# Kernel tuning notes

Hardware: AMD Instinct MI355X
Metric: run time of the kernel (lower is better)

The kernel has to match this reference:

```python
import jax, jax.numpy as jnp
import numpy as np

B, T, D_MODEL = 2, 2048, 2048
H, HD = 16, 128          # num_heads, head_dim
KV_L, Q_L, R = 512, 1024, 64  # kv_latent, q_latent, qk_rope_dim


def apply_rope(x, freqs):
    # x: (..., T, R); freqs: (T, R//2) angles theta (torch stores exp(i*theta))
    # torch pairs consecutive elements: view(..., R//2, 2) as complex
    xr = x.reshape(x.shape[:-1] + (R // 2, 2))
    x0, x1 = xr[..., 0], xr[..., 1]
    cos, sin = jnp.cos(freqs), jnp.sin(freqs)  # broadcast over leading dims
    y0 = x0 * cos - x1 * sin
    y1 = x0 * sin + x1 * cos
    return jnp.stack([y0, y1], axis=-1).reshape(x.shape)


def setup_inputs() -> dict:
    key = jax.random.key(0)
    ks = jax.random.split(key, 10)
    s = 0.02
    return {
        "x": jax.random.normal(ks[0], (B, T, D_MODEL), jnp.float32),
        "freqs": jax.random.normal(ks[1], (T, R // 2), jnp.float32),
        # weights stored as (in, out) so forward is x @ W (== torch x @ W.T)
        "W_DKV": jax.random.normal(ks[2], (D_MODEL, KV_L), jnp.float32) * s,
        "W_UK": jax.random.normal(ks[3], (KV_L, H * HD), jnp.float32) * s,
        "W_UV": jax.random.normal(ks[4], (KV_L, H * HD), jnp.float32) * s,
        "W_KR": jax.random.normal(ks[5], (D_MODEL, R), jnp.float32) * s,
        "W_DQ": jax.random.normal(ks[6], (D_MODEL, Q_L), jnp.float32) * s,
        "W_UQ": jax.random.normal(ks[7], (Q_L, H * HD), jnp.float32) * s,
        "W_QR": jax.random.normal(ks[8], (Q_L, H * R), jnp.float32) * s,
        "W_O": jax.random.normal(ks[9], (H * HD, D_MODEL), jnp.float32) * s,
    }


def reference(x, freqs, W_DKV, W_UK, W_UV, W_KR, W_DQ, W_UQ, W_QR, W_O):
    b, t, _ = x.shape
    # compressed KV latent and expansions
    c_KV = x @ W_DKV                                             # (B,T,KV_L)
    K_c = (c_KV @ W_UK).reshape(b, t, H, HD).transpose(0, 2, 1, 3)  # (B,H,T,HD)
    V = (c_KV @ W_UV).reshape(b, t, H, HD).transpose(0, 2, 1, 3)    # (B,H,T,HD)
    # shared (single-head) rope key
    K_r1 = apply_rope((x @ W_KR)[:, None, :, :], freqs)          # (B,1,T,R)
    K_r = jnp.broadcast_to(K_r1, (b, H, t, R))
    # compressed Q latent
    c_Q = x @ W_DQ                                               # (B,T,Q_L)
    Q_c = (c_Q @ W_UQ).reshape(b, t, H, HD).transpose(0, 2, 1, 3)
    Q_r = apply_rope((c_Q @ W_QR).reshape(b, t, H, R).transpose(0, 2, 1, 3), freqs)
    Q = jnp.concatenate([Q_c, Q_r], axis=-1)                     # (B,H,T,HD+R)
    K = jnp.concatenate([K_c, K_r], axis=-1)
    # causal SDPA, scale = 1/sqrt(HD+R) (torch default: query last dim)
    scale = 1.0 / jnp.sqrt(jnp.asarray(HD + R, Q.dtype))
    scores = jnp.einsum("bhqe,bhke->bhqk", Q, K) * scale
    causal = jnp.tril(jnp.ones((t, t), bool))
    scores = jnp.where(causal, scores, jnp.asarray(-1e30, scores.dtype))
    attn = jax.nn.softmax(scores, axis=-1)
    out = jnp.einsum("bhqk,bhkd->bhqd", attn, V)                 # (B,H,T,HD)
    out = out.transpose(0, 2, 1, 3).reshape(b, t, H * HD)
    y = out @ W_O                                                # (B,T,D_MODEL)
    return (y, c_KV, K_r1[:, 0, :, :])
```

## Files before the change

kernel.cpp:

```cpp
#include <hip/hip_runtime.h>
#include <stdint.h>

typedef unsigned short u16;
typedef __attribute__((ext_vector_type(8))) short s16x8;
typedef __attribute__((ext_vector_type(4))) float f32x4;

#define B_   2
#define T_   2048
#define DM   2048
#define H_   16
#define HD_  128
#define R_   64
#define E_   192
#define SCALE2 0.104117542f

__device__ __forceinline__ u16 f2b(float f) {
  union { float f; uint32_t u; } x; x.f = f;
  uint32_t u = x.u;
  return (u16)((u + 0x7FFFu + ((u >> 16) & 1u)) >> 16);
}
__device__ __forceinline__ float b2f(u16 h) {
  union { uint32_t u; float f; } x; x.u = ((uint32_t)h) << 16;
  return x.f;
}
__device__ __forceinline__ unsigned pk2(float a, float b) {
  union { float f; unsigned u; } A, B; A.f = a; B.f = b;
  return (B.u & 0xFFFF0000u) | (A.u >> 16);
}
__device__ __forceinline__ void ld_lds16(const void* g, void* l) {
  __builtin_amdgcn_global_load_lds((const __attribute__((address_space(1))) void*)g,
                                   (__attribute__((address_space(3))) void*)l,
                                   16, 0, 0);
}

__device__ __forceinline__ void conv_dev(const float* __restrict__ in, u16* __restrict__ out, int i) {
  float4 v = *(const float4*)(in + (size_t)i * 4);
  ushort4 o;
  o.x = f2b(v.x); o.y = f2b(v.y); o.z = f2b(v.z); o.w = f2b(v.w);
  *(ushort4*)(out + (size_t)i * 4) = o;
}
__device__ __forceinline__ void tr64(const float* __restrict__ in, u16* __restrict__ out,
                                     int K, int N, int bx, int by) {
  __shared__ u16 t[64][65];
  int bn = bx * 64, bk = by * 64;
  int tid = threadIdx.x;
  int r0 = tid >> 4, c0 = (tid & 15) * 4;
#pragma unroll
  for (int rr = 0; rr < 64; rr += 16) {
    float4 v = *(const float4*)(in + (size_t)(bk + r0 + rr) * N + bn + c0);
    t[r0 + rr][c0 + 0] = f2b(v.x); t[r0 + rr][c0 + 1] = f2b(v.y);
    t[r0 + rr][c0 + 2] = f2b(v.z); t[r0 + rr][c0 + 3] = f2b(v.w);
  }
  __syncthreads();
#pragma unroll
  for (int rr = 0; rr < 64; rr += 16) {
    ushort4 v;
    v.x = t[c0 + 0][r0 + rr]; v.y = t[c0 + 1][r0 + rr];
    v.z = t[c0 + 2][r0 + rr]; v.w = t[c0 + 3][r0 + rr];
    *(ushort4*)(out + (size_t)(bn + r0 + rr) * K + bk + c0) = v;
  }
}

__global__ __launch_bounds__(256)
void ta_k(const float* __restrict__ x, const float* __restrict__ fr,
          u16* __restrict__ x_bf, u16* __restrict__ fr_bf,
          const float* __restrict__ wdkv, const float* __restrict__ wkr,
          const float* __restrict__ wdq, u16* __restrict__ W) {
  int id = blockIdx.x;
  if (id < 8192)        conv_dev(x, x_bf, id * 256 + threadIdx.x);
  else if (id < 8256)   conv_dev(fr, fr_bf, (id - 8192) * 256 + threadIdx.x);
  else if (id < 8512) { int i = id - 8256; tr64(wdkv, W, 2048, 512, i & 7, i >> 3); }
  else if (id < 8544) { int i = id - 8512; tr64(wkr, W + 512 * 2048, 2048, 64, 0, i); }
  else                { int i = id - 8544; tr64(wdq, W + 576 * 2048, 2048, 1024, i & 15, i >> 4); }
}
__global__ __launch_bounds__(256)
void tb1_k(const float* __restrict__ wuk, const float* __restrict__ wuv, u16* __restrict__ W) {
  int id = blockIdx.x;
  if (id < 256) tr64(wuk, W, 512, 2048, id & 31, id >> 5);
  else { int i = id - 256; tr64(wuv, W + 2048 * 512, 512, 2048, i & 31, i >> 5); }
}
__global__ __launch_bounds__(256)
void tb2_k(const float* __restrict__ wuq, const float* __restrict__ wqr, u16* __restrict__ W) {
  int id = blockIdx.x;
  if (id < 512) tr64(wuq, W, 1024, 2048, id & 31, id >> 5);
  else { int i = id - 512; tr64(wqr, W + 2048 * 1024, 1024, 1024, i & 15, i >> 4); }
}
__global__ __launch_bounds__(256)
void tc_k(const float* __restrict__ wo, u16* __restrict__ W) {
  tr64(wo, W, 2048, 2048, blockIdx.x & 31, blockIdx.x >> 5);
}

template <int EPI>
__global__ __launch_bounds__(256)
void gemm_bf16(const u16* __restrict__ A, const u16* __restrict__ Bt,
               u16* __restrict__ O0, u16* __restrict__ O1, u16* __restrict__ O2,
               float* __restrict__ OF, float* __restrict__ OF2,
               const u16* __restrict__ FR, int M, int N, int K) {
  __shared__ __align__(16) u16 Al[128 * 32];
  __shared__ __align__(16) u16 Bl[128 * 32];
  const int tid = threadIdx.x;
  const int ln = tid & 63, w = tid >> 6;
  const int quad = ln >> 4, l16 = ln & 15;
  const int wm = (w >> 1) * 64, wn = (w & 1) * 64;
  const int m0 = blockIdx.y * 128, n0 = blockIdx.x * 128;

  f32x4 zz = {0.f, 0.f, 0.f, 0.f};
  f32x4 acc[4][4];
#pragma unroll
  for (int i = 0; i < 4; i++)
#pragma unroll
    for (int j = 0; j < 4; j++) acc[i][j] = zz;

  const u16* aG[2];
  const u16* bG[2];
  int ldsC[2];
#pragma unroll
  for (int r = 0; r < 2; r++) {
    int i = tid + r * 256;
    int row = i >> 2, cq = (i & 3) * 8;
    aG[r] = A + (size_t)(m0 + row) * K + cq;
    int rb = n0 + row;
    if (rb > N - 1) rb = N - 1;
    bG[r] = Bt + (size_t)rb * K + cq;
    ldsC[r] = ((tid & ~63) + r * 256) * 8;
  }

  for (int k = 0; k < K; k += 32) {
#pragma unroll
    for (int r = 0; r < 2; r++) {
      ld_lds16(aG[r] + k, &Al[ldsC[r]]);
      ld_lds16(bG[r] + k, &Bl[ldsC[r]]);
    }
    __syncthreads();
    s16x8 af[4], bf[4];
#pragma unroll
    for (int f = 0; f < 4; f++)
      af[f] = *(const s16x8*)&Al[(wm + f * 16 + l16) * 32 + quad * 8];
#pragma unroll
    for (int f = 0; f < 4; f++)
      bf[f] = *(const s16x8*)&Bl[(wn + f * 16 + l16) * 32 + quad * 8];
#pragma unroll
    for (int i = 0; i < 4; i++)
#pragma unroll
      for (int j = 0; j < 4; j++)
        acc[i][j] = __builtin_amdgcn_mfma_f32_16x16x32_bf16(af[i], bf[j], acc[i][j], 0, 0, 0);
    __syncthreads();
  }

#pragma unroll
  for (int fm = 0; fm < 4; fm++) {
#pragma unroll
    for (int fn = 0; fn < 4; fn++) {
      int n = n0 + wn + fn * 16 + l16;
      int mb = m0 + wm + fm * 16 + quad * 4;
      if (EPI == 2) {
        if (n < N) {
#pragma unroll
          for (int rg = 0; rg < 4; rg++) OF[(size_t)(mb + rg) * N + n] = acc[fm][fn][rg];
        }
      } else if (EPI == 4) {
        if (n < 2048) {
#pragma unroll
          for (int rg = 0; rg < 4; rg++) O0[(size_t)(mb + rg) * 2048 + n] = f2b(acc[fm][fn][rg]);
        } else {
          int hd = n - 2048, b = mb >> 11, t = mb & 2047;
          ushort4 v;
          v.x = f2b(acc[fm][fn][0]); v.y = f2b(acc[fm][fn][1]);
          v.z = f2b(acc[fm][fn][2]); v.w = f2b(acc[fm][fn][3]);
          *(ushort4*)(O1 + ((size_t)(b * 2048 + hd) * 2048 + t)) = v;
        }
      } else if (EPI == 5) {
        if (n < 2048) {
#pragma unroll
          for (int rg = 0; rg < 4; rg++) O0[(size_t)(mb + rg) * 2048 + n] = f2b(acc[fm][fn][rg]);
        } else {
#pragma unroll
          for (int rg = 0; rg < 4; rg++) O1[(size_t)(mb + rg) * 1024 + (n - 2048)] = f2b(acc[fm][fn][rg]);
        }
      } else {
        if (n < 512) {
#pragma unroll
          for (int rg = 0; rg < 4; rg++) {
            float v = acc[fm][fn][rg];
            O0[(size_t)(mb + rg) * 512 + n] = f2b(v);
            OF[(size_t)(mb + rg) * 512 + n] = v;
          }
        } else if (n < 576) {
          int r = n - 512, r2 = r >> 1, odd = r & 1;
#pragma unroll
          for (int rg = 0; rg < 4; rg++) {
            float v = acc[fm][fn][rg];
            float p = __shfl_xor(v, 1);
            int t = mb + rg;
            float a = b2f(FR[(size_t)(t & 2047) * 32 + r2]);
            float sn, cs;
            __sincosf(a, &sn, &cs);
            float y = odd ? (p * sn + v * cs) : (v * cs - p * sn);
            O1[(size_t)t * 64 + r] = f2b(y);
            OF2[(size_t)t * 64 + r] = y;
          }
        } else if (n < 1600) {
#pragma unroll
          for (int rg = 0; rg < 4; rg++) O2[(size_t)(mb + rg) * 1024 + (n - 576)] = f2b(acc[fm][fn][rg]);
        }
      }
    }
  }
}

#define KT_S 200
#define VT_S 72
#define PS_S 72
__global__ __launch_bounds__(256, 2)
void flash_attn(const u16* __restrict__ Qc, const u16* __restrict__ Qr,
                const u16* __restrict__ Kc, const u16* __restrict__ Kr,
                const u16* __restrict__ VT, const u16* __restrict__ fr,
                u16* __restrict__ O) {
  __shared__ __align__(16) u16 Kt[64 * KT_S];
  __shared__ __align__(16) u16 Vt[144 * VT_S];
  __shared__ __align__(16) u16 Ps[4][16 * PS_S];

  const int tid = threadIdx.x;
  const int ln = tid & 63, w = tid >> 6;
  const int quad = ln >> 4, l16 = ln & 15;
  const int bh = blockIdx.x, b = bh >> 4, h = bh & 15;

  for (int i = tid; i < 1024; i += 256) Vt[(128 + (i >> 6)) * VT_S + (i & 63)] = 0x3F80;

  const u16* kBase[6]; int kStep[6], kLds[6];
#pragma unroll
  for (int r = 0; r < 6; r++) {
    int i = tid + r * 256;
    int key = i / 24, c = i - key * 24;
    kLds[r] = key * KT_S + c * 8;
    if (c < 16) { kBase[r] = Kc + ((size_t)(b * T_ + key) * DM + h * HD_ + c * 8); kStep[r] = 64 * DM; }
    else        { kBase[r] = Kr + ((size_t)(b * T_ + key) * R_ + (c - 16) * 8);    kStep[r] = 64 * R_; }
  }
  const u16* vBase[4]; int vLds[4];
#pragma unroll
  for (int r = 0; r < 4; r++) {
    int i = tid + r * 256;
    vLds[r] = (i >> 3) * VT_S + (i & 7) * 8;
    vBase[r] = VT + ((size_t)(bh * HD_ + (i >> 3)) * T_ + (i & 7) * 8);
  }

  f32x4 zz = {0.f, 0.f, 0.f, 0.f};
  const int xs0 = blockIdx.y, xs1 = 31 - (int)blockIdx.y;

  for (int tt = 0; tt < 2; tt++) {
    const int q0 = (tt ? xs1 : xs0) * 64;
    const int qw = q0 + w * 16;

    s16x8 qf[6];
    {
      int t = qw + l16;
      const u16* p = Qc + ((size_t)(b * T_ + t) * DM + h * HD_ + quad * 8);
#pragma unroll
      for (int f = 0; f < 4; f++) qf[f] = *(const s16x8*)(p + f * 32);
      const u16* pr = Qr + ((size_t)(b * T_ + t) * (H_ * R_) + h * R_ + quad * 8);
#pragma unroll
      for (int half = 0; half < 2; half++) {
        s16x8 v = *(const s16x8*)(pr + half * 32);
        s16x8 o2;
#pragma unroll
        for (int p2 = 0; p2 < 4; p2++) {
          float a = b2f(fr[t * 32 + half * 16 + quad * 4 + p2]);
          float sn, cs;
          __sincosf(a, &sn, &cs);
          float x0 = b2f((u16)v[2 * p2]), x1 = b2f((u16)v[2 * p2 + 1]);
          o2[2 * p2] = (short)f2b(x0 * cs - x1 * sn);
          o2[2 * p2 + 1] = (short)f2b(x0 * sn + x1 * cs);
        }
        qf[4 + half] = o2;
      }
    }

    f32x4 o[9];
#pragma unroll
    for (int f = 0; f < 9; f++) o[f] = zz;
    float mL = -1e30f;

    const u16* pk[6]; const u16* pv[4];
    s16x8 kv[6], vv[4];
#pragma unroll
    for (int r = 0; r < 6; r++) { pk[r] = kBase[r]; kv[r] = *(const s16x8*)pk[r]; }
#pragma unroll
    for (int r = 0; r < 4; r++) { pv[r] = vBase[r]; vv[r] = *(const s16x8*)pv[r]; }

    const int nk = q0 + 64;
    for (int k0 = 0; k0 < nk; k0 += 64) {
      __syncthreads();
#pragma unroll
      for (int r = 0; r < 6; r++) *(s16x8*)&Kt[kLds[r]] = kv[r];
#pragma unroll
      for (int r = 0; r < 4; r++) *(s16x8*)&Vt[vLds[r]] = vv[r];
      __syncthreads();
      if (k0 + 64 < nk) {
#pragma unroll
        for (int r = 0; r < 6; r++) { pk[r] += kStep[r]; kv[r] = *(const s16x8*)pk[r]; }
#pragma unroll
        for (int r = 0; r < 4; r++) { pv[r] += 64; vv[r] = *(const s16x8*)pv[r]; }
      }

      f32x4 s[4];
#pragma unroll
      for (int kg = 0; kg < 4; kg++) s[kg] = zz;
#pragma unroll
      for (int e = 0; e < 6; e++)
#pragma unroll
        for (int kg = 0; kg < 4; kg++) {
          s16x8 kf = *(const s16x8*)&Kt[(kg * 16 + l16) * KT_S + e * 32 + quad * 8];
          s[kg] = __builtin_amdgcn_mfma_f32_16x16x32_bf16(kf, qf[e], s[kg], 0, 0, 0);
        }
      const int q = qw + l16;
      float sv[16];
      if (k0 + 63 <= qw) {
#pragma unroll
        for (int kg = 0; kg < 4; kg++)
#pragma unroll
          for (int rg = 0; rg < 4; rg++) sv[kg * 4 + rg] = s[kg][rg] * SCALE2;
      } else {
#pragma unroll
        for (int kg = 0; kg < 4; kg++)
#pragma unroll
          for (int rg = 0; rg < 4; rg++) {
            int key = k0 + kg * 16 + quad * 4 + rg;
            sv[kg * 4 + rg] = (key > q) ? -1e30f : s[kg][rg] * SCALE2;
          }
      }
      float mx = sv[0];
#pragma unroll
      for (int j = 1; j < 16; j++) mx = fmaxf(mx, sv[j]);
      mx = fmaxf(mx, __shfl_xor(mx, 16));
      mx = fmaxf(mx, __shfl_xor(mx, 32));
      if (__any(mx > mL)) {
        float mn = fmaxf(mL, mx);
        float alpha = exp2f(mL - mn);
        mL = mn;
        float al[4];
#pragma unroll
        for (int rg = 0; rg < 4; rg++) al[rg] = __shfl(alpha, (ln & 48) | (quad * 4 + rg));
#pragma unroll
        for (int f = 0; f < 9; f++)
#pragma unroll
          for (int rg = 0; rg < 4; rg++) o[f][rg] *= al[rg];
      }
      float p[16];
#pragma unroll
      for (int j = 0; j < 16; j++) p[j] = exp2f(sv[j] - mL);
#pragma unroll
      for (int kg = 0; kg < 4; kg++) {
        uint2 t2;
        t2.x = pk2(p[kg * 4 + 0], p[kg * 4 + 1]);
        t2.y = pk2(p[kg * 4 + 2], p[kg * 4 + 3]);
        *(uint2*)&Ps[w][l16 * PS_S + kg * 16 + quad * 4] = t2;
      }
      __asm__ volatile("s_waitcnt lgkmcnt(0)" ::: "memory");
      s16x8 pa0 = *(const s16x8*)&Ps[w][l16 * PS_S + quad * 8];
      s16x8 pa1 = *(const s16x8*)&Ps[w][l16 * PS_S + 32 + quad * 8];
#pragma unroll
      for (int f = 0; f < 9; f++) {
        s16x8 vb0 = *(const s16x8*)&Vt[(f * 16 + l16) * VT_S + quad * 8];
        o[f] = __builtin_amdgcn_mfma_f32_16x16x32_bf16(pa0, vb0, o[f], 0, 0, 0);
        s16x8 vb1 = *(const s16x8*)&Vt[(f * 16 + l16) * VT_S + 32 + quad * 8];
        o[f] = __builtin_amdgcn_mfma_f32_16x16x32_bf16(pa1, vb1, o[f], 0, 0, 0);
      }
    }

    float inv[4];
#pragma unroll
    for (int rg = 0; rg < 4; rg++) inv[rg] = 1.0f / o[8][rg];
#pragma unroll
    for (int f = 0; f < 8; f++) {
#pragma unroll
      for (int rg = 0; rg < 4; rg++) {
        int qq = qw + quad * 4 + rg;
        O[(size_t)(b * T_ + qq) * DM + h * HD_ + f * 16 + l16] = f2b(o[f][rg] * inv[rg]);
      }
    }
  }
}

extern "C" void kernel_launch(void* const* d_in, const int* in_sizes, int n_in,
                              void* d_out, int out_size, void* d_ws, size_t ws_size,
                              hipStream_t stream) {
  const float* x    = (const float*)d_in[0];
  const float* fr   = (const float*)d_in[1];
  const float* wdkv = (const float*)d_in[2];
  const float* wuk  = (const float*)d_in[3];
  const float* wuv  = (const float*)d_in[4];
  const float* wkr  = (const float*)d_in[5];
  const float* wdq  = (const float*)d_in[6];
  const float* wuq  = (const float*)d_in[7];
  const float* wqr  = (const float*)d_in[8];
  const float* wo   = (const float*)d_in[9];
  u16* ws = (u16*)d_ws;

  const int M1 = 1048576;
  u16* x_bf  = ws;
  u16* Om    = ws;
  u16* Kc    = ws + 8 * M1;
  u16* VTm   = ws + 16 * M1;
  u16* Qc    = ws + 24 * M1;
  u16* Qr    = ws + 32 * M1;
  u16* W     = ws + 36 * M1;
  u16* cKV   = ws + 40 * M1;
  u16* cQ    = ws + 42 * M1;
  u16* fr_bf = ws + 46 * M1;
  u16* kr_bf = fr_bf + 65536;

  float* out_y   = (float*)d_out;
  float* out_ckv = (float*)d_out + 8388608;
  float* out_kr  = (float*)d_out + 10485760;
  (void)in_sizes; (void)n_in; (void)out_size; (void)ws_size;

  dim3 blk(256);

  ta_k<<<dim3(9056), blk, 0, stream>>>(x, fr, x_bf, fr_bf, wdkv, wkr, wdq, W);
  gemm_bf16<6><<<dim3(13, 32), blk, 0, stream>>>(x_bf, W, cKV, kr_bf, cQ, out_ckv, out_kr, fr_bf,
                                                 4096, 1600, 2048);
  tb1_k<<<dim3(512), blk, 0, stream>>>(wuk, wuv, W);
  gemm_bf16<4><<<dim3(32, 32), blk, 0, stream>>>(cKV, W, Kc, VTm, nullptr, nullptr, nullptr, nullptr,
                                                 4096, 4096, 512);
  tb2_k<<<dim3(768), blk, 0, stream>>>(wuq, wqr, W);
  gemm_bf16<5><<<dim3(24, 32), blk, 0, stream>>>(cQ, W, Qc, Qr, nullptr, nullptr, nullptr, nullptr,
                                                 4096, 3072, 1024);
  flash_attn<<<dim3(32, 16), blk, 0, stream>>>(Qc, Qr, Kc, kr_bf, VTm, fr_bf, Om);
  tc_k<<<dim3(1024), blk, 0, stream>>>(wo, W);
  gemm_bf16<2><<<dim3(16, 32), blk, 0, stream>>>(Om, W, nullptr, nullptr, nullptr, out_y, nullptr,
                                                 nullptr, 4096, 2048, 2048);
}
```

Measured before the change: 431.4 us.

## Feed P from registers by permuting V layout; one q-tile per block

Drops the per-wave LDS staging of the softmax probabilities. The V tile is stored in shared memory with a permuted column order, so the packed P registers from the score MFMA can be used directly as the A operand of the PV MFMA. The grid is doubled so each block handles a single query tile instead of a balanced pair of tiles. Launch bounds are raised to 3 blocks per CU to increase occupancy. This removes LDS round-trips and a wait per iteration, but gives up the paired causal load balancing and adds register pressure.

After: 492.8 us. +14.2%, slower.

```diff
diff --git a/kernel.cpp b/kernel.cpp
--- a/kernel.cpp
+++ b/kernel.cpp
@@ -210,15 +210,13 @@
 
 #define KT_S 200
 #define VT_S 72
-#define PS_S 72
-__global__ __launch_bounds__(256, 2)
+__global__ __launch_bounds__(256, 3)
 void flash_attn(const u16* __restrict__ Qc, const u16* __restrict__ Qr,
                 const u16* __restrict__ Kc, const u16* __restrict__ Kr,
                 const u16* __restrict__ VT, const u16* __restrict__ fr,
                 u16* __restrict__ O) {
   __shared__ __align__(16) u16 Kt[64 * KT_S];
   __shared__ __align__(16) u16 Vt[144 * VT_S];
-  __shared__ __align__(16) u16 Ps[4][16 * PS_S];
 
   const int tid = threadIdx.x;
   const int ln = tid & 63, w = tid >> 6;
@@ -240,143 +238,144 @@
 #pragma unroll
   for (int r = 0; r < 4; r++) {
     int i = tid + r * 256;
-    vLds[r] = (i >> 3) * VT_S + (i & 7) * 8;
-    vBase[r] = VT + ((size_t)(bh * HD_ + (i >> 3)) * T_ + (i & 7) * 8);
+    int row = i >> 3, c = i & 7, c2 = c & 3;
+    vLds[r] = row * VT_S + (c >> 2) * 32 + ((2 * c2) & 3) * 8 + (c2 >> 1) * 4;
+    vBase[r] = VT + ((size_t)(bh * HD_ + row) * T_ + c * 8);
   }
 
   f32x4 zz = {0.f, 0.f, 0.f, 0.f};
-  const int xs0 = blockIdx.y, xs1 = 31 - (int)blockIdx.y;
-
-  for (int tt = 0; tt < 2; tt++) {
-    const int q0 = (tt ? xs1 : xs0) * 64;
-    const int qw = q0 + w * 16;
-
-    s16x8 qf[6];
-    {
-      int t = qw + l16;
-      const u16* p = Qc + ((size_t)(b * T_ + t) * DM + h * HD_ + quad * 8);
-#pragma unroll
-      for (int f = 0; f < 4; f++) qf[f] = *(const s16x8*)(p + f * 32);
-      const u16* pr = Qr + ((size_t)(b * T_ + t) * (H_ * R_) + h * R_ + quad * 8);
-#pragma unroll
-      for (int half = 0; half < 2; half++) {
-        s16x8 v = *(const s16x8*)(pr + half * 32);
-        s16x8 o2;
-#pragma unroll
-        for (int p2 = 0; p2 < 4; p2++) {
-          float a = b2f(fr[t * 32 + half * 16 + quad * 4 + p2]);
-          float sn, cs;
-          __sincosf(a, &sn, &cs);
-          float x0 = b2f((u16)v[2 * p2]), x1 = b2f((u16)v[2 * p2 + 1]);
-          o2[2 * p2] = (short)f2b(x0 * cs - x1 * sn);
-          o2[2 * p2 + 1] = (short)f2b(x0 * sn + x1 * cs);
+  const int q0 = (31 - (int)blockIdx.y) * 64;
+  const int qw = q0 + w * 16;
+
+  s16x8 qf[6];
+  {
+    int t = qw + l16;
+    const u16* p = Qc + ((size_t)(b * T_ + t) * DM + h * HD_ + quad * 8);
+#pragma unroll
+    for (int f = 0; f < 4; f++) qf[f] = *(const s16x8*)(p + f * 32);
+    const u16* pr = Qr + ((size_t)(b * T_ + t) * (H_ * R_) + h * R_ + quad * 8);
+#pragma unroll
+    for (int half = 0; half < 2; half++) {
+      s16x8 v = *(const s16x8*)(pr + half * 32);
+      s16x8 o2;
+#pragma unroll
+      for (int p2 = 0; p2 < 4; p2++) {
+        float a = b2f(fr[t * 32 + half * 16 + quad * 4 + p2]);
+        float sn, cs;
+        __sincosf(a, &sn, &cs);
+        float x0 = b2f((u16)v[2 * p2]), x1 = b2f((u16)v[2 * p2 + 1]);
+        o2[2 * p2] = (short)f2b(x0 * cs - x1 * sn);
+        o2[2 * p2 + 1] = (short)f2b(x0 * sn + x1 * cs);
+      }
+      qf[4 + half] = o2;
+    }
+  }
+
+  f32x4 o[9];
+#pragma unroll
+  for (int f = 0; f < 9; f++) o[f] = zz;
+  float mL = -1e30f;
+
+  const u16* pk[6]; const u16* pv[4];
+  s16x8 kv[6], vv[4];
+#pragma unroll
+  for (int r = 0; r < 6; r++) { pk[r] = kBase[r]; kv[r] = *(const s16x8*)pk[r]; }
+#pragma unroll
+  for (int r = 0; r < 4; r++) { pv[r] = vBase[r]; vv[r] = *(const s16x8*)pv[r]; }
+
+  const int nk = q0 + 64;
+  for (int k0 = 0; k0 < nk; k0 += 64) {
+    __syncthreads();
+#pragma unroll
+    for (int r = 0; r < 6; r++) *(s16x8*)&Kt[kLds[r]] = kv[r];
+#pragma unroll
+    for (int r = 0; r < 4; r++) {
+      union { s16x8 v; uint4 u; } V_; V_.v = vv[r];
+      uint2 lo; lo.x = V_.u.x; lo.y = V_.u.y;
+      uint2 hi; hi.x = V_.u.z; hi.y = V_.u.w;
+      *(uint2*)&Vt[vLds[r]] = lo;
+      *(uint2*)&Vt[vLds[r] + 8] = hi;
+    }
+    __syncthreads();
+    if (k0 + 64 < nk) {
+#pragma unroll
+      for (int r = 0; r < 6; r++) { pk[r] += kStep[r]; kv[r] = *(const s16x8*)pk[r]; }
+#pragma unroll
+      for (int r = 0; r < 4; r++) { pv[r] += 64; vv[r] = *(const s16x8*)pv[r]; }
+    }
+
+    f32x4 s[4];
+#pragma unroll
+    for (int kg = 0; kg < 4; kg++) s[kg] = zz;
+#pragma unroll
+    for (int e = 0; e < 6; e++)
+#pragma unroll
+      for (int kg = 0; kg < 4; kg++) {
+        s16x8 kf = *(const s16x8*)&Kt[(kg * 16 + l16) * KT_S + e * 32 + quad * 8];
+        s[kg] = __builtin_amdgcn_mfma_f32_16x16x32_bf16(kf, qf[e], s[kg], 0, 0, 0);
+      }
+    const int q = qw + l16;
+    float sv[16];
+    if (k0 + 63 <= qw) {
+#pragma unroll
+      for (int kg = 0; kg < 4; kg++)
+#pragma unroll
+        for (int rg = 0; rg < 4; rg++) sv[kg * 4 + rg] = s[kg][rg] * SCALE2;
+    } else {
+#pragma unroll
+      for (int kg = 0; kg < 4; kg++)
+#pragma unroll
+        for (int rg = 0; rg < 4; rg++) {
+          int key = k0 + kg * 16 + quad * 4 + rg;
+          sv[kg * 4 + rg] = (key > q) ? -1e30f : s[kg][rg] * SCALE2;
         }
-        qf[4 + half] = o2;
-      }
-    }
-
-    f32x4 o[9];
-#pragma unroll
-    for (int f = 0; f < 9; f++) o[f] = zz;
-    float mL = -1e30f;
-
-    const u16* pk[6]; const u16* pv[4];
-    s16x8 kv[6], vv[4];
-#pragma unroll
-    for (int r = 0; r < 6; r++) { pk[r] = kBase[r]; kv[r] = *(const s16x8*)pk[r]; }
-#pragma unroll
-    for (int r = 0; r < 4; r++) { pv[r] = vBase[r]; vv[r] = *(const s16x8*)pv[r]; }
-
-    const int nk = q0 + 64;
-    for (int k0 = 0; k0 < nk; k0 += 64) {
-      __syncthreads();
-#pragma unroll
-      for (int r = 0; r < 6; r++) *(s16x8*)&Kt[kLds[r]] = kv[r];
-#pragma unroll
-      for (int r = 0; r < 4; r++) *(s16x8*)&Vt[vLds[r]] = vv[r];
-      __syncthreads();
-      if (k0 + 64 < nk) {
-#pragma unroll
-        for (int r = 0; r < 6; r++) { pk[r] += kStep[r]; kv[r] = *(const s16x8*)pk[r]; }
-#pragma unroll
-        for (int r = 0; r < 4; r++) { pv[r] += 64; vv[r] = *(const s16x8*)pv[r]; }
-      }
-
-      f32x4 s[4];
-#pragma unroll
-      for (int kg = 0; kg < 4; kg++) s[kg] = zz;
-#pragma unroll
-      for (int e = 0; e < 6; e++)
-#pragma unroll
-        for (int kg = 0; kg < 4; kg++) {
-          s16x8 kf = *(const s16x8*)&Kt[(kg * 16 + l16) * KT_S + e * 32 + quad * 8];
-          s[kg] = __builtin_amdgcn_mfma_f32_16x16x32_bf16(kf, qf[e], s[kg], 0, 0, 0);
-        }
-      const int q = qw + l16;
-      float sv[16];
-      if (k0 + 63 <= qw) {
-#pragma unroll
-        for (int kg = 0; kg < 4; kg++)
-#pragma unroll
-          for (int rg = 0; rg < 4; rg++) sv[kg * 4 + rg] = s[kg][rg] * SCALE2;
-      } else {
-#pragma unroll
-        for (int kg = 0; kg < 4; kg++)
-#pragma unroll
-          for (int rg = 0; rg < 4; rg++) {
-            int key = k0 + kg * 16 + quad * 4 + rg;
-            sv[kg * 4 + rg] = (key > q) ? -1e30f : s[kg][rg] * SCALE2;
-          }
-      }
-      float mx = sv[0];
-#pragma unroll
-      for (int j = 1; j < 16; j++) mx = fmaxf(mx, sv[j]);
-      mx = fmaxf(mx, __shfl_xor(mx, 16));
-      mx = fmaxf(mx, __shfl_xor(mx, 32));
-      if (__any(mx > mL)) {
-        float mn = fmaxf(mL, mx);
-        float alpha = exp2f(mL - mn);
-        mL = mn;
-        float al[4];
-#pragma unroll
-        for (int rg = 0; rg < 4; rg++) al[rg] = __shfl(alpha, (ln & 48) | (quad * 4 + rg));
-#pragma unroll
-        for (int f = 0; f < 9; f++)
-#pragma unroll
-          for (int rg = 0; rg < 4; rg++) o[f][rg] *= al[rg];
-      }
-      float p[16];
-#pragma unroll
-      for (int j = 0; j < 16; j++) p[j] = exp2f(sv[j] - mL);
-#pragma unroll
-      for (int kg = 0; kg < 4; kg++) {
-        uint2 t2;
-        t2.x = pk2(p[kg * 4 + 0], p[kg * 4 + 1]);
-        t2.y = pk2(p[kg * 4 + 2], p[kg * 4 + 3]);
-        *(uint2*)&Ps[w][l16 * PS_S + kg * 16 + quad * 4] = t2;
-      }
-      __asm__ volatile("s_waitcnt lgkmcnt(0)" ::: "memory");
-      s16x8 pa0 = *(const s16x8*)&Ps[w][l16 * PS_S + quad * 8];
-      s16x8 pa1 = *(const s16x8*)&Ps[w][l16 * PS_S + 32 + quad * 8];
-#pragma unroll
-      for (int f = 0; f < 9; f++) {
-        s16x8 vb0 = *(const s16x8*)&Vt[(f * 16 + l16) * VT_S + quad * 8];
-        o[f] = __builtin_amdgcn_mfma_f32_16x16x32_bf16(pa0, vb0, o[f], 0, 0, 0);
-        s16x8 vb1 = *(const s16x8*)&Vt[(f * 16 + l16) * VT_S + 32 + quad * 8];
-        o[f] = __builtin_amdgcn_mfma_f32_16x16x32_bf16(pa1, vb1, o[f], 0, 0, 0);
-      }
-    }
-
-    float inv[4];
-#pragma unroll
-    for (int rg = 0; rg < 4; rg++) inv[rg] = 1.0f / o[8][rg];
-#pragma unroll
-    for (int f = 0; f < 8; f++) {
-#pragma unroll
-      for (int rg = 0; rg < 4; rg++) {
-        int qq = qw + quad * 4 + rg;
-        O[(size_t)(b * T_ + qq) * DM + h * HD_ + f * 16 + l16] = f2b(o[f][rg] * inv[rg]);
-      }
+    }
+    float mxa = fmaxf(fmaxf(sv[0], sv[1]), fmaxf(sv[2], sv[3]));
+    float mxb = fmaxf(fmaxf(sv[4], sv[5]), fmaxf(sv[6], sv[7]));
+    float mxc = fmaxf(fmaxf(sv[8], sv[9]), fmaxf(sv[10], sv[11]));
+    float mxd = fmaxf(fmaxf(sv[12], sv[13]), fmaxf(sv[14], sv[15]));
+    float mx = fmaxf(fmaxf(mxa, mxb), fmaxf(mxc, mxd));
+    mx = fmaxf(mx, __shfl_xor(mx, 16));
+    mx = fmaxf(mx, __shfl_xor(mx, 32));
+    if (__any(mx > mL)) {
+      float mn = fmaxf(mL, mx);
+      float alpha = exp2f(mL - mn);
+      mL = mn;
+      float al[4];
+#pragma unroll
+      for (int rg = 0; rg < 4; rg++) al[rg] = __shfl(alpha, (ln & 48) | (quad * 4 + rg));
+#pragma unroll
+      for (int f = 0; f < 9; f++)
+#pragma unroll
+        for (int rg = 0; rg < 4; rg++) o[f][rg] *= al[rg];
+    }
+    float p[16];
+#pragma unroll
+    for (int j = 0; j < 16; j++) p[j] = exp2f(sv[j] - mL);
+    union { unsigned pw[8]; s16x8 pa[2]; } P_;
+#pragma unroll
+    for (int kg = 0; kg < 4; kg++) {
+      P_.pw[kg * 2 + 0] = pk2(p[kg * 4 + 0], p[kg * 4 + 1]);
+      P_.pw[kg * 2 + 1] = pk2(p[kg * 4 + 2], p[kg * 4 + 3]);
+    }
+#pragma unroll
+    for (int f = 0; f < 9; f++) {
+      s16x8 vb0 = *(const s16x8*)&Vt[(f * 16 + l16) * VT_S + quad * 8];
+      o[f] = __builtin_amdgcn_mfma_f32_16x16x32_bf16(P_.pa[0], vb0, o[f], 0, 0, 0);
+      s16x8 vb1 = *(const s16x8*)&Vt[(f * 16 + l16) * VT_S + 32 + quad * 8];
+      o[f] = __builtin_amdgcn_mfma_f32_16x16x32_bf16(P_.pa[1], vb1, o[f], 0, 0, 0);
+    }
+  }
+
+  float inv[4];
+#pragma unroll
+  for (int rg = 0; rg < 4; rg++) inv[rg] = 1.0f / o[8][rg];
+#pragma unroll
+  for (int f = 0; f < 8; f++) {
+#pragma unroll
+    for (int rg = 0; rg < 4; rg++) {
+      int qq = qw + quad * 4 + rg;
+      O[(size_t)(b * T_ + qq) * DM + h * HD_ + f * 16 + l16] = f2b(o[f][rg] * inv[rg]);
     }
   }
 }
@@ -425,7 +424,7 @@
   tb2_k<<<dim3(768), blk, 0, stream>>>(wuq, wqr, W);
   gemm_bf16<5><<<dim3(24, 32), blk, 0, stream>>>(cQ, W, Qc, Qr, nullptr, nullptr, nullptr, nullptr,
                                                  4096, 3072, 1024);
-  flash_attn<<<dim3(32, 16), blk, 0, stream>>>(Qc, Qr, Kc, kr_bf, VTm, fr_bf, Om);
+  flash_attn<<<dim3(32, 32), blk, 0, stream>>>(Qc, Qr, Kc, kr_bf, VTm, fr_bf, Om);
   tc_k<<<dim3(1024), blk, 0, stream>>>(wo, W);
   gemm_bf16<2><<<dim3(16, 32), blk, 0, stream>>>(Om, W, nullptr, nullptr, nullptr, out_y, nullptr,
                                                  nullptr, 4096, 2048, 2048);
```
